# Kernel tuning notes

Measured on AMD Instinct MI355X. Metric: run time of the kernel, lower is better.

## Reference

```python
import jax, jax.numpy as jnp
import numpy as np

TOP_K = 2
CAP_FACTOR = 1.25
MIN_CAPACITY = 4


def setup_inputs() -> dict:
    key = jax.random.key(0)
    k1, k2, k3, k4 = jax.random.split(key, 4)
    B, T, C, E = 8, 2048, 1024, 8
    x = jax.random.normal(k1, (B, T, C), dtype=jnp.float32)
    w_g = jax.random.normal(k2, (E, C), dtype=jnp.float32) * 0.02   # router gate (Linear, no bias)
    c_fc = jax.random.normal(k3, (E, C, 4 * C), dtype=jnp.float32) * 0.02
    c_proj = jax.random.normal(k4, (E, 4 * C, C), dtype=jnp.float32) * 0.02
    return {"x": x, "w_g": w_g, "c_fc": c_fc, "c_proj": c_proj}


def reference(x, w_g, c_fc, c_proj):
    B, T, C = x.shape
    E = w_g.shape[0]
    N = B * T
    capacity = max(MIN_CAPACITY, int(CAP_FACTOR * N * TOP_K / E))  # 5120, static

    xf = x.reshape(N, C)
    # ---- Router (eval path: no noise, no aux losses) ----
    logits = xf @ w_g.T                                   # [N, E]
    top_logits, top_idx = jax.lax.top_k(logits, TOP_K)    # [N, k]
    router_probs = jax.nn.softmax(top_logits, axis=-1)    # [N, k]

    # position in expert: cumsum over (k-major, token) flattened order
    oh = jax.nn.one_hot(top_idx, E, dtype=jnp.int32)      # [N, k, E]
    oh_t = oh.transpose(1, 0, 2).reshape(TOP_K * N, E)
    pos = jnp.cumsum(oh_t, axis=0).reshape(TOP_K, N, E).transpose(1, 0, 2)  # [N, k, E]
    rank = jnp.sum((pos - 1) * oh, axis=-1)               # [N, k], 0-based slot in expert buffer
    valid = rank < capacity                               # capacity mask
    probs_masked = router_probs * valid.astype(router_probs.dtype)
    rank_c = jnp.clip(rank, 0, capacity - 1)

    # ---- Dispatch: scatter tokens into [E, capacity, C] buffers ----
    contrib = xf[:, None, :] * valid[..., None].astype(xf.dtype)  # [N, k, C]
    buf = jnp.zeros((E, capacity, C), dtype=xf.dtype).at[top_idx, rank_c].add(contrib)

    # ---- Experts: bmm -> ReLU^2 -> bmm ----
    h = jnp.einsum('ecd,edf->ecf', buf, c_fc)             # [E, cap, 4C]
    h = jnp.square(jax.nn.relu(h))
    expert_out = jnp.einsum('ecf,efd->ecd', h, c_proj)    # [E, cap, C]

    # ---- Combine: gather expert outputs back, weight by router probs ----
    gathered = expert_out[top_idx, rank_c]                # [N, k, C]
    out = jnp.sum(gathered * probs_masked[..., None], axis=1)
    return out.reshape(B, T, C)
```

## Files before the change

### kernel.cpp

```cpp
#include <hip/hip_runtime.h>

#define NE 8
#define CAP 5120
#define NT 16384
#define CD 1024
#define FCD 4096

typedef __attribute__((ext_vector_type(8))) short short8;
typedef __attribute__((ext_vector_type(4))) float f32x4;

__device__ __forceinline__ unsigned short f2bf(float f) {
  unsigned int u = __builtin_bit_cast(unsigned int, f);
  u += 0x7FFFu + ((u >> 16) & 1u);
  return (unsigned short)(u >> 16);
}
__device__ __forceinline__ float bf2f(unsigned short u) {
  unsigned int v = ((unsigned int)u) << 16;
  return __builtin_bit_cast(float, v);
}
__device__ __forceinline__ void g2lds16(const unsigned short* g, unsigned short* l) {
  __builtin_amdgcn_global_load_lds(
      (const __attribute__((address_space(1))) unsigned int*)(unsigned long long)g,
      (__attribute__((address_space(3))) unsigned int*)l,
      16, 0, 0);
}

__global__ __launch_bounds__(256) void fill_i32_k(int* __restrict__ p, int v, int n) {
  int i = blockIdx.x * 256 + threadIdx.x;
  if (i < n) p[i] = v;
}
__global__ __launch_bounds__(256) void fill_zero_f32x4_k(float4* __restrict__ p, size_t n4) {
  size_t i = (size_t)blockIdx.x * 256 + threadIdx.x;
  if (i < n4) p[i] = make_float4(0.f, 0.f, 0.f, 0.f);
}

__global__ __launch_bounds__(256) void transpose_bf16_k(
    const float* __restrict__ in, unsigned short* __restrict__ out, int R, int Cc) {
  __shared__ float tile[64][65];
  const size_t esz = (size_t)R * Cc;
  const float* inp = in + (size_t)blockIdx.z * esz;
  unsigned short* outp = out + (size_t)blockIdx.z * esz;
  const int cbase = blockIdx.x * 64, rbase = blockIdx.y * 64;
  const int t = threadIdx.x;
#pragma unroll
  for (int i = 0; i < 4; ++i) {
    int idx = i * 256 + t;
    int r = idx >> 4, c4 = (idx & 15) * 4;
    const float4 v = *reinterpret_cast<const float4*>(inp + (size_t)(rbase + r) * Cc + cbase + c4);
    tile[r][c4 + 0] = v.x; tile[r][c4 + 1] = v.y; tile[r][c4 + 2] = v.z; tile[r][c4 + 3] = v.w;
  }
  __syncthreads();
#pragma unroll
  for (int i = 0; i < 4; ++i) {
    int idx = i * 256 + t;
    int oc = idx >> 4, q = (idx & 15) * 4;
    ushort4 o;
    o.x = f2bf(tile[q + 0][oc]); o.y = f2bf(tile[q + 1][oc]);
    o.z = f2bf(tile[q + 2][oc]); o.w = f2bf(tile[q + 3][oc]);
    *reinterpret_cast<ushort4*>(outp + (size_t)(cbase + oc) * R + rbase + q) = o;
  }
}

__global__ __launch_bounds__(256) void router_k(
    const float* __restrict__ x, const float* __restrict__ wg,
    unsigned short* __restrict__ xb, int* __restrict__ topidx, float* __restrict__ probs) {
  __shared__ float wls[NE * CD];
  const int t = threadIdx.x;
  {
    const float4* w4 = (const float4*)wg;
    float4* l4 = (float4*)wls;
    for (int i = t; i < NE * CD / 4; i += 256) l4[i] = w4[i];
  }
  __syncthreads();
  const int wave = t >> 6, lane = t & 63;
  const int gw = blockIdx.x * 4 + wave;
  const float4* wls4 = (const float4*)wls;
#pragma unroll
  for (int it = 0; it < 2; ++it) {
    const int n = gw * 2 + it;
    const float4* xr4 = (const float4*)(x + (size_t)n * CD);
    ushort4* xb4 = (ushort4*)(xb + (size_t)n * CD);
    double acc[NE] = {0, 0, 0, 0, 0, 0, 0, 0};
#pragma unroll
    for (int j = 0; j < 4; ++j) {
      const int idx = j * 64 + lane;
      const float4 xv = xr4[idx];
      ushort4 o;
      o.x = f2bf(xv.x); o.y = f2bf(xv.y); o.z = f2bf(xv.z); o.w = f2bf(xv.w);
      xb4[idx] = o;
#pragma unroll
      for (int e = 0; e < NE; ++e) {
        const float4 wv = wls4[e * 256 + idx];
        acc[e] += (double)xv.x * (double)wv.x + (double)xv.y * (double)wv.y
                + (double)xv.z * (double)wv.z + (double)xv.w * (double)wv.w;
      }
    }
#pragma unroll
    for (int s = 32; s >= 1; s >>= 1) {
#pragma unroll
      for (int e = 0; e < NE; ++e) acc[e] += __shfl_xor(acc[e], s, 64);
    }
    if (lane == 0) {
      int i1 = 0; double v1 = acc[0];
      for (int e = 1; e < NE; ++e) if (acc[e] > v1) { v1 = acc[e]; i1 = e; }
      int i2 = -1; double v2 = -1e300;
      for (int e = 0; e < NE; ++e) if (e != i1 && acc[e] > v2) { v2 = acc[e]; i2 = e; }
      float p0 = 1.0f / (1.0f + expf((float)(v2 - v1)));
      topidx[n * 2 + 0] = i1; topidx[n * 2 + 1] = i2;
      probs[n * 2 + 0] = p0; probs[n * 2 + 1] = 1.0f - p0;
    }
  }
}

__global__ __launch_bounds__(256) void hist_k(const int* __restrict__ topidx, int* __restrict__ blkhist) {
  __shared__ int h[16];
  const int t = threadIdx.x;
  if (t < 16) h[t] = 0;
  __syncthreads();
  const int n = blockIdx.x * 256 + t;
  atomicAdd(&h[topidx[n * 2 + 0]], 1);
  atomicAdd(&h[8 + topidx[n * 2 + 1]], 1);
  __syncthreads();
  if (t < 16) blkhist[blockIdx.x * 16 + t] = h[t];
}

__global__ void scan_k(const int* __restrict__ blkhist, int* __restrict__ blkoff, int* __restrict__ totals_cnt) {
  const int t = threadIdx.x;
  if (t < 16) {
    int s = 0;
    for (int b = 0; b < 64; ++b) { blkoff[b * 16 + t] = s; s += blkhist[b * 16 + t]; }
    totals_cnt[t] = s;
  }
  __syncthreads();
  if (t < 8) {
    int tot = totals_cnt[t] + totals_cnt[8 + t];
    totals_cnt[16 + t] = tot < CAP ? tot : CAP;
  }
}

__global__ __launch_bounds__(256) void rank_k(
    const int* __restrict__ topidx, const int* __restrict__ blkoff,
    const int* __restrict__ totals_cnt, int* __restrict__ ranks, int* __restrict__ slotmap) {
  __shared__ int wcnt[2][4][8];
  __shared__ int woff[2][4][8];
  const int t = threadIdx.x, wave = t >> 6, lane = t & 63;
  const int n = blockIdx.x * 256 + t;
  const int e1 = topidx[n * 2 + 0], e2 = topidx[n * 2 + 1];
  const unsigned long long lt = (1ull << lane) - 1ull;
  int pre1 = 0, pre2 = 0;
#pragma unroll
  for (int e = 0; e < 8; ++e) {
    unsigned long long m1 = __ballot(e1 == e);
    unsigned long long m2 = __ballot(e2 == e);
    if (e1 == e) pre1 = __popcll(m1 & lt);
    if (e2 == e) pre2 = __popcll(m2 & lt);
    if (lane == 0) { wcnt[0][wave][e] = __popcll(m1); wcnt[1][wave][e] = __popcll(m2); }
  }
  __syncthreads();
  if (t < 16) {
    int k = t >> 3, e = t & 7, s = 0;
    for (int w = 0; w < 4; ++w) { woff[k][w][e] = s; s += wcnt[k][w][e]; }
  }
  __syncthreads();
  int r1 = blkoff[blockIdx.x * 16 + e1] + woff[0][wave][e1] + pre1;
  int r2 = totals_cnt[e2] + blkoff[blockIdx.x * 16 + 8 + e2] + woff[1][wave][e2] + pre2;
  ranks[n * 2 + 0] = (r1 < CAP) ? r1 : -1;
  ranks[n * 2 + 1] = (r2 < CAP) ? r2 : -1;
  if (r1 < CAP) slotmap[e1 * CAP + r1] = n * 2 + 0;
  if (r2 < CAP) slotmap[e2 * CAP + r2] = n * 2 + 1;
}

template <int BM, int TN>
__device__ __forceinline__ bool map_tile(const int* cnt, int e_base, int n_le,
                                         int& le, int& mt, int& nt) {
  constexpr int TM = CAP / BM;
  int pref[9];
  int L = 0;
  for (int i = 0; i < n_le; ++i) {
    pref[i] = L;
    int lm = (cnt[e_base + i] + BM - 1) / BM;
    if (lm > TM) lm = TM;
    L += lm;
  }
  const int totalLive = L * TN;
  const int bid = blockIdx.x;
  if (bid >= totalLive) return false;
  const int q = totalLive >> 3, r = totalLive & 7;
  const int xcd = bid & 7, lin = bid >> 3;
  const int wid = (xcd < r ? xcd * (q + 1) : r * (q + 1) + (xcd - r) * q) + lin;
  const int pair = wid / TN;
  nt = wid % TN;
  le = n_le - 1;
  for (int i = 1; i < n_le; ++i) if (pair < pref[i]) { le = i - 1; break; }
  mt = pair - pref[le];
  return true;
}

template <int BM, int KDIM, int NDIM, bool GATHER, bool RELU2>
__global__ __launch_bounds__(512) void gemm8p_k(
    const unsigned short* __restrict__ A, const unsigned short* __restrict__ Bt,
    unsigned short* __restrict__ Out, const int* __restrict__ slotmap,
    const int* __restrict__ cnt, int e_base, int n_le) {
  constexpr int BN = 256;
  constexpr int KT = KDIM / 64;
  constexpr int TN = NDIM / BN;
  constexpr int M_REP = BM / 32;
  constexpr int QM = M_REP / 2;
  constexpr int AL = BM / 128;
  constexpr int BL = 2;
  constexpr int V = AL + BL;

  __shared__ unsigned short lA[2][BM * 64];
  __shared__ unsigned short lB[2][BN * 64];

  int le, mt, nt;
  if (!map_tile<BM, TN>(cnt, e_base, n_le, le, mt, nt)) return;
  const int e = e_base + le;

  const int tid = threadIdx.x;
  const int wave = tid >> 6, lane = tid & 63;
  const int wr = wave >> 2, wc = wave & 3;
  const int l15 = lane & 15, l4 = lane >> 4;

  const unsigned short* sApt[2][AL];
  const unsigned short* sBpt[2][BL];
#pragma unroll
  for (int h = 0; h < 2; ++h) {
#pragma unroll
    for (int j = 0; j < AL; ++j) {
      const int lc = j * 512 + tid;
      const int lr = lc >> 3, pc = lc & 7;
      const int logc = pc ^ (lr & 7);
      const int rowT = h * (BM / 2) + lr;
      size_t grow;
      if (GATHER) {
        const int sv = slotmap[e * CAP + mt * BM + rowT];
        grow = (size_t)(sv < 0 ? 0 : (sv >> 1));
      } else {
        grow = (size_t)le * CAP + mt * BM + rowT;
      }
      sApt[h][j] = A + grow * KDIM + logc * 8;
    }
#pragma unroll
    for (int j = 0; j < BL; ++j) {
      const int lc = j * 512 + tid;
      const int lr = lc >> 3, pc = lc & 7;
      const int logc = pc ^ (lr & 7);
      sBpt[h][j] = Bt + ((size_t)le * NDIM + nt * BN + h * 128 + lr) * KDIM + logc * 8;
    }
  }

#define STAGE_A(sl, h, tt)                                                              \
  do { _Pragma("unroll") for (int j = 0; j < AL; ++j)                                   \
    g2lds16(sApt[h][j] + (size_t)(tt) * 64,                                             \
            &lA[sl][((h) * (BM / 2) * 8 + j * 512 + wave * 64) * 8]); } while (0)
#define STAGE_B(sl, h, tt)                                                              \
  do { _Pragma("unroll") for (int j = 0; j < BL; ++j)                                   \
    g2lds16(sBpt[h][j] + (size_t)(tt) * 64,                                             \
            &lB[sl][((h) * 128 * 8 + j * 512 + wave * 64) * 8]); } while (0)

  const int kidx0 = ((0 * 4 + l4) ^ (l15 & 7)) * 8;
  const int kidx1 = ((1 * 4 + l4) ^ (l15 & 7)) * 8;

#define RD_A(mh)                                                                        \
  do { _Pragma("unroll") for (int m = 0; m < QM; ++m) {                                 \
    const int row = (mh) * (BM / 2) + wr * (BM / 4) + m * 16 + l15;                     \
    aF[m][0] = *(const short8*)(bA + row * 64 + kidx0);                                 \
    aF[m][1] = *(const short8*)(bA + row * 64 + kidx1); } } while (0)
#define RD_B(DST, nh)                                                                   \
  do { _Pragma("unroll") for (int n = 0; n < 2; ++n) {                                  \
    const int row = (nh) * 128 + wc * 32 + n * 16 + l15;                                \
    DST[n][0] = *(const short8*)(bB + row * 64 + kidx0);                                \
    DST[n][1] = *(const short8*)(bB + row * 64 + kidx1); } } while (0)
#define LGK0()                                                                          \
  do { asm volatile("s_waitcnt lgkmcnt(0)" ::: "memory");                               \
       __builtin_amdgcn_sched_barrier(0); } while (0)
#define MF(BARR, mh, nh)                                                                \
  do { __builtin_amdgcn_s_setprio(1);                                                   \
    _Pragma("unroll") for (int m = 0; m < QM; ++m)                                      \
      _Pragma("unroll") for (int n = 0; n < 2; ++n) {                                   \
        acc[(mh) * QM + m][(nh) * 2 + n] = __builtin_amdgcn_mfma_f32_16x16x32_bf16(     \
            aF[m][0], BARR[n][0], acc[(mh) * QM + m][(nh) * 2 + n], 0, 0, 0);           \
        acc[(mh) * QM + m][(nh) * 2 + n] = __builtin_amdgcn_mfma_f32_16x16x32_bf16(     \
            aF[m][1], BARR[n][1], acc[(mh) * QM + m][(nh) * 2 + n], 0, 0, 0); }         \
    __builtin_amdgcn_s_setprio(0); } while (0)
#define VMC_V()  do { if constexpr (V == 4) asm volatile("s_waitcnt vmcnt(4)" ::: "memory"); \
                      else asm volatile("s_waitcnt vmcnt(3)" ::: "memory"); } while (0)
#define VMC_2()  asm volatile("s_waitcnt vmcnt(2)" ::: "memory")
#define VMC_0()  asm volatile("s_waitcnt vmcnt(0)" ::: "memory")
#define BAR()    do { __builtin_amdgcn_s_barrier(); asm volatile("" ::: "memory"); } while (0)

  f32x4 acc[M_REP][4] = {};
  short8 aF[QM][2], bF0[2][2], bF1[2][2];

  STAGE_A(0, 0, 0); STAGE_B(0, 0, 0); STAGE_B(0, 1, 0); STAGE_A(0, 1, 0);
  VMC_V();
  BAR();

  int s = 0;
  for (int t = 0; t < KT; ++t) {
    const int s2 = s ^ 1;
    const unsigned short* bA = &lA[s][0];
    const unsigned short* bB = &lB[s][0];
    const bool more = (t + 1 < KT);

    RD_A(0); RD_B(bF0, 0);
    if (more) { STAGE_A(s2, 0, t + 1); VMC_V(); } else { VMC_2(); }
    LGK0();
    MF(bF0, 0, 0);
    BAR();
    RD_B(bF1, 1);
    if (more) { STAGE_B(s2, 0, t + 1); VMC_V(); } else { VMC_0(); }
    LGK0();
    MF(bF1, 0, 1);
    BAR();
    RD_A(1);
    if (more) STAGE_B(s2, 1, t + 1);
    LGK0();
    MF(bF1, 1, 1);
    if (more) { STAGE_A(s2, 1, t + 1); VMC_V(); }
    MF(bF0, 1, 0);
    if (more) BAR();
    s = s2;
  }

  const size_t rowb = (size_t)le * CAP + mt * BM;
  const int colb = nt * BN;
#pragma unroll
  for (int i = 0; i < M_REP; ++i) {
    const int mh = i / QM, m = i % QM;
#pragma unroll
    for (int j = 0; j < 4; ++j) {
      const int nh = j / 2, n = j % 2;
#pragma unroll
      for (int rr = 0; rr < 4; ++rr) {
        float v = acc[i][j][rr];
        if (RELU2) { v = fmaxf(v, 0.0f); v = v * v; }
        const size_t orow = rowb + mh * (BM / 2) + wr * (BM / 4) + m * 16 + l4 * 4 + rr;
        Out[orow * NDIM + colb + nh * 128 + wc * 32 + n * 16 + l15] = f2bf(v);
      }
    }
  }
#undef STAGE_A
#undef STAGE_B
#undef RD_A
#undef RD_B
#undef LGK0
#undef MF
#undef VMC_V
#undef VMC_2
#undef VMC_0
#undef BAR
}

template <int WM, int WN, int BM, int BN, int KDIM, int NDIM, bool GATHER, bool RELU2, bool SCATTER>
__global__ __launch_bounds__(WM * WN * 64) void gemm8_k(
    const unsigned short* __restrict__ A, const unsigned short* __restrict__ Bt,
    unsigned short* __restrict__ Out, const int* __restrict__ slotmap,
    const int* __restrict__ cnt, int e_base, int n_le,
    const float* __restrict__ probs, float* __restrict__ outp) {
  constexpr int THREADS = WM * WN * 64;
  constexpr int KT = KDIM / 32;
  constexpr int TN = NDIM / BN;
  constexpr int M_REP = BM / WM / 16;
  constexpr int N_REP = BN / WN / 16;
  constexpr int MH = M_REP / 2;
  constexpr int ALOADS = BM * 4 / THREADS;
  constexpr int BLOADS = BN * 4 / THREADS;
  static_assert(ALOADS + BLOADS == 4, "vmcnt literal assumes 4 loads/wave/tile");

  __shared__ unsigned short lA[3][BM * 32];
  __shared__ unsigned short lB[3][BN * 32];

  int le, mt, nt;
  if (!map_tile<BM, TN>(cnt, e_base, n_le, le, mt, nt)) return;
  const int e = e_base + le;

  const int tid = threadIdx.x;
  const int wave = tid >> 6, lane = tid & 63;
  const int wr = wave / WN, wc = wave % WN;
  const int l15 = lane & 15, l4 = lane >> 4;

  const unsigned short* pA[ALOADS];
  const unsigned short* pB[BLOADS];
#pragma unroll
  for (int j = 0; j < ALOADS; ++j) {
    const int ci = j * THREADS + tid;
    const int row = ci >> 2, cst = ci & 3;
    const int csrc = cst ^ ((row >> 1) & 3);
    size_t grow;
    if (GATHER) {
      const int sv = slotmap[e * CAP + mt * BM + row];
      grow = (size_t)(sv < 0 ? 0 : (sv >> 1));
    } else {
      grow = (size_t)le * CAP + mt * BM + row;
    }
    pA[j] = A + grow * KDIM + csrc * 8;
  }
#pragma unroll
  for (int j = 0; j < BLOADS; ++j) {
    const int ci = j * THREADS + tid;
    const int row = ci >> 2, cst = ci & 3;
    const int csrc = cst ^ ((row >> 1) & 3);
    pB[j] = Bt + ((size_t)le * NDIM + nt * BN + row) * KDIM + csrc * 8;
  }

  const int ksw = (l4 ^ ((l15 >> 1) & 3)) * 8;
  int aOff[M_REP], bOff[N_REP];
#pragma unroll
  for (int m = 0; m < M_REP; ++m)
    aOff[m] = (wr * (BM / WM) + m * 16 + l15) * 32 + ksw;
#pragma unroll
  for (int n = 0; n < N_REP; ++n)
    bOff[n] = (wc * (BN / WN) + n * 16 + l15) * 32 + ksw;

  f32x4 acc[M_REP][N_REP] = {};

#pragma unroll
  for (int kt = 0; kt < 2; ++kt) {
#pragma unroll
    for (int j = 0; j < ALOADS; ++j)
      g2lds16(pA[j] + kt * 32, &lA[kt][(j * THREADS + wave * 64) * 8]);
#pragma unroll
    for (int j = 0; j < BLOADS; ++j)
      g2lds16(pB[j] + kt * 32, &lB[kt][(j * THREADS + wave * 64) * 8]);
  }

  for (int t = 0; t < KT; ++t) {
    if (t < KT - 1) asm volatile("s_waitcnt vmcnt(4)" ::: "memory");
    else            asm volatile("s_waitcnt vmcnt(0)" ::: "memory");
    __builtin_amdgcn_s_barrier();
    asm volatile("" ::: "memory");

    const int s = t % 3, s2 = (t + 2) % 3;
    const unsigned short* sA = &lA[s][0];
    const unsigned short* sB = &lB[s][0];
    const bool pf = (t + 2 < KT);

    short8 aF[MH], bF[N_REP];
#pragma unroll
    for (int m = 0; m < MH; ++m) aF[m] = *(const short8*)(sA + aOff[m]);
#pragma unroll
    for (int n = 0; n < N_REP; ++n) bF[n] = *(const short8*)(sB + bOff[n]);
    if (pf) {
#pragma unroll
      for (int j = 0; j < ALOADS; ++j)
        g2lds16(pA[j] + (t + 2) * 32, &lA[s2][(j * THREADS + wave * 64) * 8]);
    }
    asm volatile("s_waitcnt lgkmcnt(0)" ::: "memory");
    __builtin_amdgcn_sched_barrier(0);
    __builtin_amdgcn_s_setprio(1);
#pragma unroll
    for (int m = 0; m < MH; ++m)
#pragma unroll
      for (int n = 0; n < N_REP; ++n)
        acc[m][n] = __builtin_amdgcn_mfma_f32_16x16x32_bf16(aF[m], bF[n], acc[m][n], 0, 0, 0);
    __builtin_amdgcn_s_setprio(0);

    short8 aG[MH];
#pragma unroll
    for (int m = 0; m < MH; ++m) aG[m] = *(const short8*)(sA + aOff[MH + m]);
    if (pf) {
#pragma unroll
      for (int j = 0; j < BLOADS; ++j)
        g2lds16(pB[j] + (t + 2) * 32, &lB[s2][(j * THREADS + wave * 64) * 8]);
    }
    asm volatile("s_waitcnt lgkmcnt(0)" ::: "memory");
    __builtin_amdgcn_sched_barrier(0);
    __builtin_amdgcn_s_setprio(1);
#pragma unroll
    for (int m = 0; m < MH; ++m)
#pragma unroll
      for (int n = 0; n < N_REP; ++n)
        acc[MH + m][n] = __builtin_amdgcn_mfma_f32_16x16x32_bf16(aG[m], bF[n], acc[MH + m][n], 0, 0, 0);
    __builtin_amdgcn_s_setprio(0);
  }

  if (SCATTER) {
    const int colb = nt * BN + wc * (BN / WN);
#pragma unroll
    for (int m = 0; m < M_REP; ++m) {
#pragma unroll
      for (int rr = 0; rr < 4; ++rr) {
        const int rl = mt * BM + wr * (BM / WM) + m * 16 + l4 * 4 + rr;
        const int sv = slotmap[e * CAP + rl];
        if (sv < 0) continue;
        const float p = probs[sv];
        float* ob = outp + (size_t)(sv >> 1) * CD + colb + l15;
#pragma unroll
        for (int n = 0; n < N_REP; ++n)
          atomicAdd(&ob[n * 16], p * acc[m][n][rr]);
      }
    }
  } else {
    const size_t rowb = (size_t)le * CAP + mt * BM + wr * (BM / WM);
    const int colb = nt * BN + wc * (BN / WN);
#pragma unroll
    for (int m = 0; m < M_REP; ++m)
#pragma unroll
      for (int n = 0; n < N_REP; ++n)
#pragma unroll
        for (int rr = 0; rr < 4; ++rr) {
          float v = acc[m][n][rr];
          if (RELU2) { v = fmaxf(v, 0.0f); v = v * v; }
          Out[(rowb + m * 16 + l4 * 4 + rr) * NDIM + colb + n * 16 + l15] = f2bf(v);
        }
  }
}

extern "C" void kernel_launch(void* const* d_in, const int* in_sizes, int n_in,
                              void* d_out, int out_size, void* d_ws, size_t ws_size,
                              hipStream_t stream) {
  const float* x = (const float*)d_in[0];
  const float* wg = (const float*)d_in[1];
  const float* cfc = (const float*)d_in[2];
  const float* cproj = (const float*)d_in[3];
  float* out = (float*)d_out;
  char* ws = (char*)d_ws;
  (void)in_sizes; (void)n_in; (void)out_size;

  const size_t W1SZ = (size_t)FCD * CD * 2;
  const size_t HSZ  = (size_t)CAP * FCD * 2;

  size_t off = 0;
  auto alloc = [&](size_t bytes) { size_t o = off; off = (off + bytes + 255) & ~(size_t)255; return o; };
  unsigned short* XB = (unsigned short*)(ws + alloc((size_t)NT * CD * 2));
  int* TOPIDX  = (int*)(ws + alloc((size_t)NT * 2 * 4));
  float* PROBS = (float*)(ws + alloc((size_t)NT * 2 * 4));
  int* RANKS   = (int*)(ws + alloc((size_t)NT * 2 * 4));
  int* SLOTMAP = (int*)(ws + alloc((size_t)NE * CAP * 4));
  int* BLKHIST = (int*)(ws + alloc(64 * 16 * 4));
  int* BLKOFF  = (int*)(ws + alloc(64 * 16 * 4));
  int* TOTALS  = (int*)(ws + alloc(256));
  const size_t shared_end = off;
  int* CNT = TOTALS + 16;

  size_t woff = shared_end;
  auto walloc = [&](size_t bytes) { size_t o = woff; woff = (woff + bytes + 255) & ~(size_t)255; return o; };
  const size_t oCFCT   = walloc(NE * W1SZ);
  const size_t oCPROJT = walloc(NE * W1SZ);
  const size_t weights_end = woff;

  int EG = 0;
  for (int g = 8; g >= 1; g >>= 1) {
    size_t need = weights_end + (size_t)g * HSZ + 512;
    if (ws_size >= need) { EG = g; break; }
  }
  if (EG == 0) {
    fill_zero_f32x4_k<<<(NT * CD / 4 + 255) / 256, 256, 0, stream>>>((float4*)out, (size_t)NT * CD / 4);
    return;
  }

  fill_i32_k<<<(NE * CAP + 255) / 256, 256, 0, stream>>>(SLOTMAP, -1, NE * CAP);
  fill_zero_f32x4_k<<<(NT * CD / 4 + 255) / 256, 256, 0, stream>>>((float4*)out, (size_t)NT * CD / 4);
  router_k<<<2048, 256, 0, stream>>>(x, wg, XB, TOPIDX, PROBS);
  hist_k<<<64, 256, 0, stream>>>(TOPIDX, BLKHIST);
  scan_k<<<1, 64, 0, stream>>>(BLKHIST, BLKOFF, TOTALS);
  rank_k<<<64, 256, 0, stream>>>(TOPIDX, BLKOFF, TOTALS, RANKS, SLOTMAP);

  unsigned short* CFCT   = (unsigned short*)(ws + oCFCT);
  unsigned short* CPROJT = (unsigned short*)(ws + oCPROJT);
  transpose_bf16_k<<<dim3(FCD / 64, CD / 64, NE), 256, 0, stream>>>(cfc, CFCT, CD, FCD);
  transpose_bf16_k<<<dim3(CD / 64, FCD / 64, NE), 256, 0, stream>>>(cproj, CPROJT, FCD, CD);

  unsigned short* H = (unsigned short*)(ws + weights_end);

  for (int g = 0; g < NE / EG; ++g) {
    const int eb = g * EG;
    gemm8p_k<256, CD, FCD, true, true>
        <<<EG * (CAP / 256) * (FCD / 256), 512, 0, stream>>>(
        XB, CFCT + (size_t)eb * FCD * CD, H, SLOTMAP, CNT, eb, EG);
    gemm8_k<2, 2, 128, 128, FCD, CD, false, false, true>
        <<<EG * (CAP / 128) * (CD / 128), 256, 0, stream>>>(
        H, CPROJT + (size_t)eb * CD * FCD, nullptr, SLOTMAP, CNT, eb, EG, PROBS, out);
  }
}
```

Measured before the change: 883.5 us.

## Replace atomic combine with direct per-slot stores and a final sum kernel

The down-projection GEMM no longer atomically adds weighted outputs into a zeroed fp32 output. First-choice contributions are stored directly to the output and second-choice contributions to a separate bf16 buffer, which aliases the activation buffer when all experts run in one group. A new sum kernel then adds the two using the ranks to tell which slots are valid. This removes the output zero-fill and the atomics in exchange for one extra pass over the output and bf16 rounding of the second contribution. It also relies on RANKS marking dropped tokens as negative and on XB being dead after the first GEMM.

```diff
diff --git a/kernel.cpp b/kernel.cpp
--- a/kernel.cpp
+++ b/kernel.cpp
@@ -358,7 +358,8 @@
     const unsigned short* __restrict__ A, const unsigned short* __restrict__ Bt,
     unsigned short* __restrict__ Out, const int* __restrict__ slotmap,
     const int* __restrict__ cnt, int e_base, int n_le,
-    const float* __restrict__ probs, float* __restrict__ outp) {
+    const float* __restrict__ probs, float* __restrict__ outp,
+    unsigned short* __restrict__ out2) {
   constexpr int THREADS = WM * WN * 64;
   constexpr int KT = KDIM / 32;
   constexpr int TN = NDIM / BN;
@@ -486,10 +487,16 @@
         const int sv = slotmap[e * CAP + rl];
         if (sv < 0) continue;
         const float p = probs[sv];
-        float* ob = outp + (size_t)(sv >> 1) * CD + colb + l15;
-#pragma unroll
-        for (int n = 0; n < N_REP; ++n)
-          atomicAdd(&ob[n * 16], p * acc[m][n][rr]);
+        const size_t tok = (size_t)(sv >> 1);
+        if (sv & 1) {
+          unsigned short* ob = out2 + tok * CD + colb + l15;
+#pragma unroll
+          for (int n = 0; n < N_REP; ++n) ob[n * 16] = f2bf(p * acc[m][n][rr]);
+        } else {
+          float* ob = outp + tok * CD + colb + l15;
+#pragma unroll
+          for (int n = 0; n < N_REP; ++n) ob[n * 16] = p * acc[m][n][rr];
+        }
       }
     }
   } else {
@@ -506,6 +513,21 @@
           Out[(rowb + m * 16 + l4 * 4 + rr) * NDIM + colb + n * 16 + l15] = f2bf(v);
         }
   }
+}
+
+__global__ __launch_bounds__(256) void sum_k(
+    const unsigned short* __restrict__ out2, const int* __restrict__ ranks,
+    float* __restrict__ out) {
+  const int n = blockIdx.x, t = threadIdx.x;
+  const int c = t * 4;
+  const int r1 = ranks[n * 2 + 0], r2 = ranks[n * 2 + 1];
+  float4 v = make_float4(0.f, 0.f, 0.f, 0.f);
+  if (r1 >= 0) v = *reinterpret_cast<const float4*>(out + (size_t)n * CD + c);
+  if (r2 >= 0) {
+    const ushort4 u = *(const ushort4*)(out2 + (size_t)n * CD + c);
+    v.x += bf2f(u.x); v.y += bf2f(u.y); v.z += bf2f(u.z); v.w += bf2f(u.w);
+  }
+  *reinterpret_cast<float4*>(out + (size_t)n * CD + c) = v;
 }
 
 extern "C" void kernel_launch(void* const* d_in, const int* in_sizes, int n_in,
@@ -521,6 +543,7 @@
 
   const size_t W1SZ = (size_t)FCD * CD * 2;
   const size_t HSZ  = (size_t)CAP * FCD * 2;
+  const size_t O2SZ = (size_t)NT * CD * 2;
 
   size_t off = 0;
   auto alloc = [&](size_t bytes) { size_t o = off; off = (off + bytes + 255) & ~(size_t)255; return o; };
@@ -542,9 +565,10 @@
   const size_t weights_end = woff;
 
   int EG = 0;
+  bool aliasO2 = false;
   for (int g = 8; g >= 1; g >>= 1) {
-    size_t need = weights_end + (size_t)g * HSZ + 512;
-    if (ws_size >= need) { EG = g; break; }
+    size_t need = weights_end + (size_t)g * HSZ + 512 + (g == 8 ? 0 : O2SZ + 512);
+    if (ws_size >= need) { EG = g; aliasO2 = (g == 8); break; }
   }
   if (EG == 0) {
     fill_zero_f32x4_k<<<(NT * CD / 4 + 255) / 256, 256, 0, stream>>>((float4*)out, (size_t)NT * CD / 4);
@@ -552,7 +576,6 @@
   }
 
   fill_i32_k<<<(NE * CAP + 255) / 256, 256, 0, stream>>>(SLOTMAP, -1, NE * CAP);
-  fill_zero_f32x4_k<<<(NT * CD / 4 + 255) / 256, 256, 0, stream>>>((float4*)out, (size_t)NT * CD / 4);
   router_k<<<2048, 256, 0, stream>>>(x, wg, XB, TOPIDX, PROBS);
   hist_k<<<64, 256, 0, stream>>>(TOPIDX, BLKHIST);
   scan_k<<<1, 64, 0, stream>>>(BLKHIST, BLKOFF, TOTALS);
@@ -564,6 +587,8 @@
   transpose_bf16_k<<<dim3(CD / 64, FCD / 64, NE), 256, 0, stream>>>(cproj, CPROJT, FCD, CD);
 
   unsigned short* H = (unsigned short*)(ws + weights_end);
+  unsigned short* OUT2 = aliasO2 ? XB
+      : (unsigned short*)(ws + ((weights_end + (size_t)EG * HSZ + 255) & ~(size_t)255));
 
   for (int g = 0; g < NE / EG; ++g) {
     const int eb = g * EG;
@@ -572,6 +597,7 @@
         XB, CFCT + (size_t)eb * FCD * CD, H, SLOTMAP, CNT, eb, EG);
     gemm8_k<2, 2, 128, 128, FCD, CD, false, false, true>
         <<<EG * (CAP / 128) * (CD / 128), 256, 0, stream>>>(
-        H, CPROJT + (size_t)eb * CD * FCD, nullptr, SLOTMAP, CNT, eb, EG, PROBS, out);
-  }
-}
+        H, CPROJT + (size_t)eb * CD * FCD, nullptr, SLOTMAP, CNT, eb, EG, PROBS, out, OUT2);
+  }
+  sum_k<<<NT, 256, 0, stream>>>(OUT2, RANKS, out);
+}
```

Measured after the change: 850.1 us (median of 2 runs). -3.8%, faster.
